# Performance work log

Hardware: AMD Instinct MI355X
Metric: run time of the kernel (lower is better)

## Reference

```python
import jax, jax.numpy as jnp
import numpy as np

N_NODES = 50000
N_EDGES = 800000
D_IN = 256
DIM_H = 256
N_GRAPHS = 500
N_OUT = 10
BN_EPS = 1e-5


def _mlp(h, W1, b1, gamma, beta, mean, var, W2, b2):
    # Linear -> BatchNorm1d (eval, running stats) -> ReLU -> Linear -> ReLU
    h = h @ W1 + b1
    h = (h - mean) * (gamma / jnp.sqrt(var + BN_EPS)) + beta
    h = jax.nn.relu(h)
    return jax.nn.relu(h @ W2 + b2)


def _gin_conv(x, src, dst, params):
    # PyG GINConv with eps=0: out = nn(x + sum_{j in N(i)} x_j)
    agg = jax.ops.segment_sum(x[src], dst, num_segments=N_NODES)
    return _mlp(x + agg, *params)


def setup_inputs() -> dict:
    key = jax.random.key(0)
    ks = jax.random.split(key, 24)
    x = jax.random.normal(ks[0], (N_NODES, D_IN), dtype=jnp.float32)
    edge_index = jax.random.randint(ks[1], (2, N_EDGES), 0, N_NODES, dtype=jnp.int64)
    batch = jnp.sort(jax.random.randint(ks[2], (N_NODES,), 0, N_GRAPHS, dtype=jnp.int64))

    def lin(k, fan_in, fan_out):
        s = 1.0 / np.sqrt(fan_in)
        kw, kb = jax.random.split(k)
        W = jax.random.uniform(kw, (fan_in, fan_out), minval=-s, maxval=s, dtype=jnp.float32)
        b = jax.random.uniform(kb, (fan_out,), minval=-s, maxval=s, dtype=jnp.float32)
        return W, b

    def bn(k, d):
        k1, k2, k3, k4 = jax.random.split(k, 4)
        gamma = 1.0 + 0.1 * jax.random.normal(k1, (d,), dtype=jnp.float32)
        beta = 0.1 * jax.random.normal(k2, (d,), dtype=jnp.float32)
        mean = 0.1 * jax.random.normal(k3, (d,), dtype=jnp.float32)
        var = jax.random.uniform(k4, (d,), minval=0.5, maxval=1.5, dtype=jnp.float32)
        return gamma, beta, mean, var

    W1a, b1a = lin(ks[3], D_IN, DIM_H)
    g1a, be1a, m1a, v1a = bn(ks[4], DIM_H)
    W2a, b2a = lin(ks[5], DIM_H, DIM_H)
    W1b, b1b = lin(ks[6], DIM_H, DIM_H)
    g1b, be1b, m1b, v1b = bn(ks[7], DIM_H)
    W2b, b2b = lin(ks[8], DIM_H, DIM_H)
    lin1_W, lin1_b = lin(ks[9], DIM_H * 2, DIM_H * 3)
    lin2_W, lin2_b = lin(ks[10], DIM_H * 3, N_OUT)

    return dict(x=x, edge_index=edge_index, batch=batch,
                W1a=W1a, b1a=b1a, g1a=g1a, be1a=be1a, m1a=m1a, v1a=v1a, W2a=W2a, b2a=b2a,
                W1b=W1b, b1b=b1b, g1b=g1b, be1b=be1b, m1b=m1b, v1b=v1b, W2b=W2b, b2b=b2b,
                lin1_W=lin1_W, lin1_b=lin1_b, lin2_W=lin2_W, lin2_b=lin2_b)


def reference(x, edge_index, batch,
              W1a, b1a, g1a, be1a, m1a, v1a, W2a, b2a,
              W1b, b1b, g1b, be1b, m1b, v1b, W2b, b2b,
              lin1_W, lin1_b, lin2_W, lin2_b):
    src, dst = edge_index[0], edge_index[1]
    h1 = _gin_conv(x, src, dst, (W1a, b1a, g1a, be1a, m1a, v1a, W2a, b2a))
    h2 = _gin_conv(h1, src, dst, (W1b, b1b, g1b, be1b, m1b, v1b, W2b, b2b))
    p1 = jax.ops.segment_sum(h1, batch, num_segments=N_GRAPHS)  # global_add_pool
    p2 = jax.ops.segment_sum(h2, batch, num_segments=N_GRAPHS)
    h = jnp.concatenate([p1, p2], axis=1)
    h = jax.nn.relu(h @ lin1_W + lin1_b)
    # dropout p=0.6 is identity in eval mode
    h = h @ lin2_W + lin2_b
    return jax.nn.log_softmax(h, axis=1)
```

## Files before the change

kernel.cpp:

```cpp
#include <hip/hip_runtime.h>

#define N_NODES 50000
#define MPAD 50176
#define N_EDGES 800000
#define DIM 256
#define N_GRAPHS 500
#define N_OUT 10
#define BN_EPS 1e-5f
#define SCAN_BS 1024
#define KSPLIT 4

typedef unsigned int u32;
typedef short bf16x8 __attribute__((ext_vector_type(8)));
typedef unsigned short us8 __attribute__((ext_vector_type(8)));
typedef float f32x4 __attribute__((ext_vector_type(4)));

typedef __attribute__((address_space(1))) const unsigned int gas_u32;
typedef __attribute__((address_space(3))) unsigned int las_u32;

__device__ inline void g2l16(const void* g, void* l) {
    __builtin_amdgcn_global_load_lds((gas_u32*)g, (las_u32*)l, 16, 0, 0);
}

__device__ inline float b2f(unsigned short u) {
    union { u32 i; float f; } c; c.i = ((u32)u) << 16; return c.f;
}
__device__ inline unsigned short f2b(float f) {
    u32 x = __builtin_bit_cast(u32, f);
    return (unsigned short)((x + 0x7FFFu + ((x >> 16) & 1u)) >> 16);
}

__global__ void zero_i(int* __restrict__ p, int n) {
    int i = blockIdx.x * blockDim.x + threadIdx.x;
    if (i < n) p[i] = 0;
}
__global__ void hist_dst(const int* __restrict__ dst, int* __restrict__ deg) {
    int e = blockIdx.x * blockDim.x + threadIdx.x;
    if (e < N_EDGES) atomicAdd(&deg[dst[e]], 1);
}
__global__ void scan_phase1(const int* __restrict__ deg, int* __restrict__ rowptr,
                            int* __restrict__ bsum, int n) {
    __shared__ int sh[SCAN_BS];
    int i = blockIdx.x * SCAN_BS + threadIdx.x;
    int v = (i < n) ? deg[i] : 0;
    sh[threadIdx.x] = v;
    __syncthreads();
    for (int off = 1; off < SCAN_BS; off <<= 1) {
        int t = (threadIdx.x >= off) ? sh[threadIdx.x - off] : 0;
        __syncthreads();
        sh[threadIdx.x] += t;
        __syncthreads();
    }
    if (i < n) rowptr[i] = sh[threadIdx.x] - v;
    if (threadIdx.x == SCAN_BS - 1) bsum[blockIdx.x] = sh[threadIdx.x];
}
__global__ void scan_phase2(int* __restrict__ bsum, int nb) {
    if (threadIdx.x == 0 && blockIdx.x == 0) {
        int run = 0;
        for (int b = 0; b < nb; b++) { int v = bsum[b]; bsum[b] = run; run += v; }
    }
}
__global__ void scan_phase3(int* __restrict__ rowptr, int* __restrict__ cursor,
                            const int* __restrict__ bsum, int n) {
    int i = blockIdx.x * SCAN_BS + threadIdx.x;
    if (i < n) {
        int v = rowptr[i] + bsum[blockIdx.x];
        rowptr[i] = v;
        cursor[i] = v;
    }
    if (i == 0) rowptr[n] = N_EDGES;
}
__global__ void fill_csr(const int* __restrict__ src, const int* __restrict__ dst,
                         int* __restrict__ cursor, int* __restrict__ col) {
    int e = blockIdx.x * blockDim.x + threadIdx.x;
    if (e < N_EDGES) {
        int p = atomicAdd(&cursor[dst[e]], 1);
        col[p] = src[e];
    }
}
__global__ void graph_starts(const int* __restrict__ batch, int* __restrict__ gstart) {
    int g = blockIdx.x * blockDim.x + threadIdx.x;
    if (g > N_GRAPHS) return;
    if (g == N_GRAPHS) { gstart[g] = N_NODES; return; }
    int lo = 0, hi = N_NODES;
    while (lo < hi) { int mid = (lo + hi) >> 1; if (batch[mid] < g) lo = mid + 1; else hi = mid; }
    gstart[g] = lo;
}

__global__ void conv_x(const float4* __restrict__ in, ushort4* __restrict__ out, int n4) {
    int i = blockIdx.x * blockDim.x + threadIdx.x;
    if (i < n4) {
        float4 v = in[i];
        ushort4 o; o.x = f2b(v.x); o.y = f2b(v.y); o.z = f2b(v.z); o.w = f2b(v.w);
        out[i] = o;
    }
}
__global__ void conv_wt4(const float* __restrict__ W0, const float* __restrict__ W1,
                         const float* __restrict__ W2, const float* __restrict__ W3,
                         unsigned short* __restrict__ Wt) {
    int mat = blockIdx.y;
    const float* W = (mat == 0) ? W0 : (mat == 1) ? W1 : (mat == 2) ? W2 : W3;
    int n = blockIdx.x;
    int k = threadIdx.x;
    Wt[((size_t)mat << 16) + (size_t)n * 256 + k] = f2b(W[(size_t)k * 256 + n]);
}
__global__ void make_ss(const float* __restrict__ bias, const float* __restrict__ gamma,
                        const float* __restrict__ beta, const float* __restrict__ mean,
                        const float* __restrict__ var, float* __restrict__ scale,
                        float* __restrict__ shift, int has_bn) {
    int i = threadIdx.x;
    if (has_bn) {
        float s = gamma[i] * rsqrtf(var[i] + BN_EPS);
        scale[i] = s;
        shift[i] = (bias[i] - mean[i]) * s + beta[i];
    } else {
        scale[i] = 1.f;
        shift[i] = bias[i];
    }
}

__global__ void gather_bf(const unsigned short* __restrict__ feat,
                          const int* __restrict__ col,
                          const int* __restrict__ rowptr,
                          unsigned short* __restrict__ out) {
    int node = blockIdx.x * 4 + (threadIdx.x >> 6);
    if (node >= N_NODES) return;
    int lane = threadIdx.x & 63;
    int half = lane >> 5;
    int d8 = (lane & 31) * 8;
    float acc[8];
    #pragma unroll
    for (int j = 0; j < 8; j++) acc[j] = 0.f;
    if (half == 0) {
        us8 own = *reinterpret_cast<const us8*>(&feat[(size_t)node * DIM + d8]);
        #pragma unroll
        for (int j = 0; j < 8; j++) acc[j] = b2f((unsigned short)own[j]);
    }
    int s = rowptr[node], e = rowptr[node + 1];
    int i = s + half;
    for (; i + 6 < e; i += 8) {
        int n0 = col[i], n1 = col[i + 2], n2 = col[i + 4], n3 = col[i + 6];
        us8 v0 = *reinterpret_cast<const us8*>(&feat[(size_t)n0 * DIM + d8]);
        us8 v1 = *reinterpret_cast<const us8*>(&feat[(size_t)n1 * DIM + d8]);
        us8 v2 = *reinterpret_cast<const us8*>(&feat[(size_t)n2 * DIM + d8]);
        us8 v3 = *reinterpret_cast<const us8*>(&feat[(size_t)n3 * DIM + d8]);
        #pragma unroll
        for (int j = 0; j < 8; j++)
            acc[j] += (b2f((unsigned short)v0[j]) + b2f((unsigned short)v1[j]))
                    + (b2f((unsigned short)v2[j]) + b2f((unsigned short)v3[j]));
    }
    for (; i < e; i += 2) {
        int n0 = col[i];
        us8 v0 = *reinterpret_cast<const us8*>(&feat[(size_t)n0 * DIM + d8]);
        #pragma unroll
        for (int j = 0; j < 8; j++) acc[j] += b2f((unsigned short)v0[j]);
    }
    #pragma unroll
    for (int j = 0; j < 8; j++) acc[j] += __shfl_xor(acc[j], 32, 64);
    if (half == 0) {
        us8 o;
        #pragma unroll
        for (int j = 0; j < 8; j++) o[j] = (short)f2b(acc[j]);
        *reinterpret_cast<us8*>(&out[(size_t)node * DIM + d8]) = o;
    }
}

__global__ __launch_bounds__(512)
void gemm_bf16(const unsigned short* __restrict__ A,
               const unsigned short* __restrict__ Wt,
               const float* __restrict__ scale,
               const float* __restrict__ shift,
               unsigned short* __restrict__ C, int M) {
    __shared__ unsigned short Asb[2][128 * 32];
    __shared__ unsigned short Bsb[2][256 * 32];
    int t = threadIdx.x;
    int wave = t >> 6, lane = t & 63;
    int m0 = blockIdx.x * 128;
    int wr = (wave >> 2) * 64;
    int wc = (wave & 3) * 64;

    int cb = (t & 3) * 16;
    const char* Ab  = (const char*)A  + (size_t)(m0 + (t >> 2)) * 512 + cb;
    const char* Bb0 = (const char*)Wt + (size_t)(t >> 2) * 512 + cb;
    const char* Bb1 = (const char*)Wt + (size_t)(128 + (t >> 2)) * 512 + cb;

    f32x4 acc[4][4];
    #pragma unroll
    for (int m = 0; m < 4; m++)
        #pragma unroll
        for (int n = 0; n < 4; n++)
            acc[m][n] = (f32x4){0.f, 0.f, 0.f, 0.f};

    int rsel = lane & 15;
    int ksel = (lane >> 4) * 8;

    #pragma unroll
    for (int p = 0; p < 2; p++) {
        size_t ko = (size_t)p * 64;
        g2l16(Ab + ko,  (char*)Asb[p] + (size_t)t * 16);
        g2l16(Bb0 + ko, (char*)Bsb[p] + (size_t)t * 16);
        g2l16(Bb1 + ko, (char*)Bsb[p] + (size_t)(512 + t) * 16);
    }

    #pragma unroll
    for (int ks = 0; ks < 8; ks++) {
        const int cur = ks & 1;
        if (ks < 7) asm volatile("s_waitcnt vmcnt(3)" ::: "memory");
        else        asm volatile("s_waitcnt vmcnt(0)" ::: "memory");
        __builtin_amdgcn_s_barrier();
        asm volatile("" ::: "memory");

        const unsigned short* As = Asb[cur];
        const unsigned short* Bs = Bsb[cur];
        bf16x8 af[4], bfr[4];
        #pragma unroll
        for (int m = 0; m < 4; m++)
            af[m] = *(const bf16x8*)&As[(size_t)(wr + m * 16 + rsel) * 32 + ksel];
        #pragma unroll
        for (int n = 0; n < 4; n++)
            bfr[n] = *(const bf16x8*)&Bs[(size_t)(wc + n * 16 + rsel) * 32 + ksel];
        #pragma unroll
        for (int m = 0; m < 4; m++)
            #pragma unroll
            for (int n = 0; n < 4; n++)
                acc[m][n] = __builtin_amdgcn_mfma_f32_16x16x32_bf16(af[m], bfr[n], acc[m][n], 0, 0, 0);

        asm volatile("" ::: "memory");
        __builtin_amdgcn_s_barrier();
        if (ks + 2 < 8) {
            size_t ko = (size_t)(ks + 2) * 64;
            g2l16(Ab + ko,  (char*)Asb[cur] + (size_t)t * 16);
            g2l16(Bb0 + ko, (char*)Bsb[cur] + (size_t)t * 16);
            g2l16(Bb1 + ko, (char*)Bsb[cur] + (size_t)(512 + t) * 16);
        }
    }

    int cr = lane >> 4;
    #pragma unroll
    for (int n = 0; n < 4; n++) {
        int colg = wc + n * 16 + rsel;
        float s = scale[colg], sh = shift[colg];
        #pragma unroll
        for (int m = 0; m < 4; m++) {
            int rowb = m0 + wr + m * 16 + cr * 4;
            #pragma unroll
            for (int r = 0; r < 4; r++) {
                int row = rowb + r;
                if (row < M) {
                    float v = fmaxf(acc[m][n][r] * s + sh, 0.f);
                    C[(size_t)row * 256 + colg] = f2b(v);
                }
            }
        }
    }
}

__global__ void pool_seg(const unsigned short* __restrict__ h1,
                         const unsigned short* __restrict__ h2,
                         const int* __restrict__ gstart,
                         float* __restrict__ pcat) {
    int g = blockIdx.x;
    int t = threadIdx.x;
    int s = gstart[g], e = gstart[g + 1];
    float a1 = 0.f, a2 = 0.f;
    for (int n = s; n < e; n++) {
        a1 += b2f(h1[(size_t)n * DIM + t]);
        a2 += b2f(h2[(size_t)n * DIM + t]);
    }
    pcat[(size_t)g * 512 + t]       = a1;
    pcat[(size_t)g * 512 + 256 + t] = a2;
}

__global__ void head1(const float* __restrict__ A,
                      const float* __restrict__ W1,
                      float* __restrict__ Hpart) {
    __shared__ float As[16][65];
    __shared__ float Bs[16][65];
    int t = threadIdx.x;
    int m0 = blockIdx.y * 64;
    int n0 = blockIdx.x * 64;
    int kz = blockIdx.z * (512 / KSPLIT);
    int tx = t & 15, ty = t >> 4;
    float acc[4][4] = {};
    for (int k0 = kz; k0 < kz + 512 / KSPLIT; k0 += 16) {
        #pragma unroll
        for (int i = 0; i < 4; i++) {
            int r = (t >> 4) + i * 16;
            int k = t & 15;
            int gr = m0 + r;
            As[k][r] = (gr < N_GRAPHS) ? A[(size_t)gr * 512 + k0 + k] : 0.f;
        }
        #pragma unroll
        for (int i = 0; i < 4; i++) {
            int k = (t >> 6) + i * 4;
            int n = t & 63;
            Bs[k][n] = W1[(size_t)(k0 + k) * 768 + n0 + n];
        }
        __syncthreads();
        #pragma unroll
        for (int k = 0; k < 16; k++) {
            float a[4], b[4];
            #pragma unroll
            for (int i = 0; i < 4; i++) a[i] = As[k][ty * 4 + i];
            #pragma unroll
            for (int j = 0; j < 4; j++) b[j] = Bs[k][tx * 4 + j];
            #pragma unroll
            for (int i = 0; i < 4; i++)
                #pragma unroll
                for (int j = 0; j < 4; j++)
                    acc[i][j] += a[i] * b[j];
        }
        __syncthreads();
    }
    float* Hz = Hpart + (size_t)blockIdx.z * N_GRAPHS * 768;
    #pragma unroll
    for (int i = 0; i < 4; i++) {
        int gm = m0 + ty * 4 + i;
        if (gm >= N_GRAPHS) continue;
        #pragma unroll
        for (int j = 0; j < 4; j++) {
            int gn = n0 + tx * 4 + j;
            Hz[(size_t)gm * 768 + gn] = acc[i][j];
        }
    }
}

__global__ void head2(const float* __restrict__ Hpart, const float* __restrict__ b1,
                      const float* __restrict__ W2, const float* __restrict__ b2,
                      float* __restrict__ out) {
    int g = blockIdx.x;
    int lane = threadIdx.x;
    float part[N_OUT];
    #pragma unroll
    for (int o = 0; o < N_OUT; o++) part[o] = 0.f;
    for (int k = lane; k < 768; k += 64) {
        float hv = b1[k];
        #pragma unroll
        for (int z = 0; z < KSPLIT; z++)
            hv += Hpart[((size_t)z * N_GRAPHS + g) * 768 + k];
        hv = fmaxf(hv, 0.f);
        #pragma unroll
        for (int o = 0; o < N_OUT; o++) part[o] += hv * W2[(size_t)k * N_OUT + o];
    }
    #pragma unroll
    for (int o = 0; o < N_OUT; o++) {
        #pragma unroll
        for (int off = 32; off > 0; off >>= 1)
            part[o] += __shfl_down(part[o], off, 64);
    }
    if (lane == 0) {
        float logits[N_OUT];
        float mx = -1e30f;
        #pragma unroll
        for (int o = 0; o < N_OUT; o++) { logits[o] = part[o] + b2[o]; mx = fmaxf(mx, logits[o]); }
        float ssum = 0.f;
        #pragma unroll
        for (int o = 0; o < N_OUT; o++) ssum += expf(logits[o] - mx);
        float lse = logf(ssum);
        #pragma unroll
        for (int o = 0; o < N_OUT; o++)
            out[(size_t)g * N_OUT + o] = logits[o] - mx - lse;
    }
}

extern "C" void kernel_launch(void* const* d_in, const int* in_sizes, int n_in,
                              void* d_out, int out_size, void* d_ws, size_t ws_size,
                              hipStream_t stream) {
    const float* x     = (const float*)d_in[0];
    const int*   ei    = (const int*)d_in[1];
    const int*   batch = (const int*)d_in[2];
    const float* W1a = (const float*)d_in[3];
    const float* b1a = (const float*)d_in[4];
    const float* g1a = (const float*)d_in[5];
    const float* be1a= (const float*)d_in[6];
    const float* m1a = (const float*)d_in[7];
    const float* v1a = (const float*)d_in[8];
    const float* W2a = (const float*)d_in[9];
    const float* b2a = (const float*)d_in[10];
    const float* W1b = (const float*)d_in[11];
    const float* b1b = (const float*)d_in[12];
    const float* g1b = (const float*)d_in[13];
    const float* be1b= (const float*)d_in[14];
    const float* m1b = (const float*)d_in[15];
    const float* v1b = (const float*)d_in[16];
    const float* W2b = (const float*)d_in[17];
    const float* b2b = (const float*)d_in[18];
    const float* lin1_W = (const float*)d_in[19];
    const float* lin1_b = (const float*)d_in[20];
    const float* lin2_W = (const float*)d_in[21];
    const float* lin2_b = (const float*)d_in[22];

    const size_t NBUF = (size_t)MPAD * DIM;
    char* ws = (char*)d_ws;
    unsigned short* agg  = (unsigned short*)ws;            ws += NBUF * 2;
    unsigned short* mid  = (unsigned short*)ws;            ws += NBUF * 2;
    unsigned short* h1   = (unsigned short*)ws;            ws += NBUF * 2;
    unsigned short* h2   = (unsigned short*)ws;            ws += NBUF * 2;
    unsigned short* x_bf = (unsigned short*)ws;            ws += (size_t)N_NODES * DIM * 2;
    unsigned short* Wt   = (unsigned short*)ws;            ws += 4 * 65536 * 2;
    float* ss    = (float*)ws;                             ws += 8 * 256 * 4;
    float* pcat  = (float*)ws;                             ws += (size_t)N_GRAPHS * 512 * 4;
    float* Hpart = (float*)ws;                             ws += (size_t)KSPLIT * N_GRAPHS * 768 * 4;
    int* deg     = (int*)ws;                               ws += (size_t)N_NODES * 4;
    int* cursor  = (int*)ws;                               ws += (size_t)N_NODES * 4;
    int* rowptr  = (int*)ws;                               ws += (size_t)(N_NODES + 1) * 4;
    int* bsum    = (int*)ws;                               ws += 64 * 4;
    int* col     = (int*)ws;                               ws += (size_t)N_EDGES * 4;
    int* gstart  = (int*)ws;

    const int* srcE = ei;
    const int* dstE = ei + N_EDGES;

    const int nscan = (N_NODES + SCAN_BS - 1) / SCAN_BS;

    zero_i<<<(N_NODES + 255) / 256, 256, 0, stream>>>(deg, N_NODES);
    hist_dst<<<(N_EDGES + 255) / 256, 256, 0, stream>>>(dstE, deg);
    scan_phase1<<<nscan, SCAN_BS, 0, stream>>>(deg, rowptr, bsum, N_NODES);
    scan_phase2<<<1, 64, 0, stream>>>(bsum, nscan);
    scan_phase3<<<nscan, SCAN_BS, 0, stream>>>(rowptr, cursor, bsum, N_NODES);
    fill_csr<<<(N_EDGES + 255) / 256, 256, 0, stream>>>(srcE, dstE, cursor, col);
    graph_starts<<<2, 256, 0, stream>>>(batch, gstart);

    conv_x<<<(N_NODES * DIM / 4 + 255) / 256, 256, 0, stream>>>(
        (const float4*)x, (ushort4*)x_bf, N_NODES * DIM / 4);
    dim3 wt_grid(256, 4);
    conv_wt4<<<wt_grid, 256, 0, stream>>>(W1a, W2a, W1b, W2b, Wt);
    make_ss<<<1, 256, 0, stream>>>(b1a, g1a, be1a, m1a, v1a, ss + 0 * 512, ss + 0 * 512 + 256, 1);
    make_ss<<<1, 256, 0, stream>>>(b2a, nullptr, nullptr, nullptr, nullptr, ss + 1 * 512, ss + 1 * 512 + 256, 0);
    make_ss<<<1, 256, 0, stream>>>(b1b, g1b, be1b, m1b, v1b, ss + 2 * 512, ss + 2 * 512 + 256, 1);
    make_ss<<<1, 256, 0, stream>>>(b2b, nullptr, nullptr, nullptr, nullptr, ss + 3 * 512, ss + 3 * 512 + 256, 0);

    gather_bf<<<(N_NODES + 3) / 4, 256, 0, stream>>>(x_bf, col, rowptr, agg);
    gemm_bf16<<<MPAD / 128, 512, 0, stream>>>(agg, Wt + 0 * 65536, ss + 0 * 512, ss + 0 * 512 + 256, mid, N_NODES);
    gemm_bf16<<<MPAD / 128, 512, 0, stream>>>(mid, Wt + 1 * 65536, ss + 1 * 512, ss + 1 * 512 + 256, h1, N_NODES);

    gather_bf<<<(N_NODES + 3) / 4, 256, 0, stream>>>(h1, col, rowptr, agg);
    gemm_bf16<<<MPAD / 128, 512, 0, stream>>>(agg, Wt + 2 * 65536, ss + 2 * 512, ss + 2 * 512 + 256, mid, N_NODES);
    gemm_bf16<<<MPAD / 128, 512, 0, stream>>>(mid, Wt + 3 * 65536, ss + 3 * 512, ss + 3 * 512 + 256, h2, N_NODES);

    pool_seg<<<N_GRAPHS, 256, 0, stream>>>(h1, h2, gstart, pcat);
    dim3 h1grid(12, 8, KSPLIT);
    head1<<<h1grid, 256, 0, stream>>>(pcat, lin1_W, Hpart);
    head2<<<N_GRAPHS, 64, 0, stream>>>(Hpart, lin1_b, lin2_W, lin2_b, (float*)d_out);
}
```

Before: 395.3 us.

## Fuse both MLP GEMMs into one kernel keeping intermediate tile in LDS

Replaces the two back-to-back GEMM launches per GIN layer with a single kernel that computes Linear+BN+ReLU into a swizzled LDS buffer, then runs the second GEMM straight from LDS. This removes the global write and re-read of the 50k x 256 intermediate activation and one launch per layer, and it prefetches the second weight matrix during the tail of the first GEMM. In exchange, tiles shrink from 128 to 64 rows with 4 waves, each block reloads both full weight matrices, and LDS use grows to about 72 KB, which may limit occupancy.

```diff
diff --git a/kernel.cpp b/kernel.cpp
--- a/kernel.cpp
+++ b/kernel.cpp
@@ -28,6 +28,10 @@
 __device__ inline unsigned short f2b(float f) {
     u32 x = __builtin_bit_cast(u32, f);
     return (unsigned short)((x + 0x7FFFu + ((x >> 16) & 1u)) >> 16);
+}
+
+__device__ inline int mid_addr(int row, int col) {
+    return row * 512 + ((((col >> 3) ^ (row & 31)) << 4) | ((col & 7) << 1));
 }
 
 __global__ void zero_i(int* __restrict__ p, int n) {
@@ -107,16 +111,11 @@
 __global__ void make_ss(const float* __restrict__ bias, const float* __restrict__ gamma,
                         const float* __restrict__ beta, const float* __restrict__ mean,
                         const float* __restrict__ var, float* __restrict__ scale,
-                        float* __restrict__ shift, int has_bn) {
+                        float* __restrict__ shift) {
     int i = threadIdx.x;
-    if (has_bn) {
-        float s = gamma[i] * rsqrtf(var[i] + BN_EPS);
-        scale[i] = s;
-        shift[i] = (bias[i] - mean[i]) * s + beta[i];
-    } else {
-        scale[i] = 1.f;
-        shift[i] = bias[i];
-    }
+    float s = gamma[i] * rsqrtf(var[i] + BN_EPS);
+    scale[i] = s;
+    shift[i] = (bias[i] - mean[i]) * s + beta[i];
 }
 
 __global__ void gather_bf(const unsigned short* __restrict__ feat,
@@ -165,24 +164,39 @@
     }
 }
 
-__global__ __launch_bounds__(512)
-void gemm_bf16(const unsigned short* __restrict__ A,
-               const unsigned short* __restrict__ Wt,
-               const float* __restrict__ scale,
-               const float* __restrict__ shift,
-               unsigned short* __restrict__ C, int M) {
-    __shared__ unsigned short Asb[2][128 * 32];
-    __shared__ unsigned short Bsb[2][256 * 32];
+__global__ __launch_bounds__(256, 2)
+void fused_mlp(const unsigned short* __restrict__ A,
+               const unsigned short* __restrict__ W1t,
+               const unsigned short* __restrict__ W2t,
+               const float* __restrict__ scale1,
+               const float* __restrict__ shift1,
+               const float* __restrict__ shift2,
+               unsigned short* __restrict__ H, int M) {
+    __shared__ __align__(16) unsigned short Asb[2][64 * 32];
+    __shared__ __align__(16) unsigned short Bsb[2][256 * 32];
+    __shared__ __align__(16) unsigned short midb[64 * 256];
+
     int t = threadIdx.x;
     int wave = t >> 6, lane = t & 63;
-    int m0 = blockIdx.x * 128;
-    int wr = (wave >> 2) * 64;
-    int wc = (wave & 3) * 64;
+    int m0 = blockIdx.x * 64;
+    int wc = wave * 64;
+    int rsel = lane & 15;
+    int ksel = (lane >> 4) * 8;
+    int cr = lane >> 4;
+
+    float s1[4], sh1[4], sh2[4];
+    #pragma unroll
+    for (int n = 0; n < 4; n++) {
+        int colg = wc + n * 16 + rsel;
+        s1[n]  = scale1[colg];
+        sh1[n] = shift1[colg];
+        sh2[n] = shift2[colg];
+    }
 
     int cb = (t & 3) * 16;
-    const char* Ab  = (const char*)A  + (size_t)(m0 + (t >> 2)) * 512 + cb;
-    const char* Bb0 = (const char*)Wt + (size_t)(t >> 2) * 512 + cb;
-    const char* Bb1 = (const char*)Wt + (size_t)(128 + (t >> 2)) * 512 + cb;
+    const char* Ab  = (const char*)A   + (size_t)(m0 + (t >> 2)) * 512 + cb;
+    const char* B1b = (const char*)W1t + (size_t)(t >> 2) * 512 + cb;
+    const char* B2b = (const char*)W2t + (size_t)(t >> 2) * 512 + cb;
 
     f32x4 acc[4][4];
     #pragma unroll
@@ -191,22 +205,20 @@
         for (int n = 0; n < 4; n++)
             acc[m][n] = (f32x4){0.f, 0.f, 0.f, 0.f};
 
-    int rsel = lane & 15;
-    int ksel = (lane >> 4) * 8;
-
     #pragma unroll
     for (int p = 0; p < 2; p++) {
         size_t ko = (size_t)p * 64;
-        g2l16(Ab + ko,  (char*)Asb[p] + (size_t)t * 16);
-        g2l16(Bb0 + ko, (char*)Bsb[p] + (size_t)t * 16);
-        g2l16(Bb1 + ko, (char*)Bsb[p] + (size_t)(512 + t) * 16);
+        g2l16(Ab + ko, (char*)Asb[p] + (size_t)t * 16);
+        #pragma unroll
+        for (int i = 0; i < 4; i++)
+            g2l16(B1b + (size_t)i * 32768 + ko, (char*)Bsb[p] + (size_t)(i * 256 + t) * 16);
     }
 
     #pragma unroll
     for (int ks = 0; ks < 8; ks++) {
         const int cur = ks & 1;
-        if (ks < 7) asm volatile("s_waitcnt vmcnt(3)" ::: "memory");
-        else        asm volatile("s_waitcnt vmcnt(0)" ::: "memory");
+        if (ks < 7) asm volatile("s_waitcnt vmcnt(5)" ::: "memory");
+        else        asm volatile("s_waitcnt vmcnt(4)" ::: "memory");
         __builtin_amdgcn_s_barrier();
         asm volatile("" ::: "memory");
 
@@ -215,7 +227,7 @@
         bf16x8 af[4], bfr[4];
         #pragma unroll
         for (int m = 0; m < 4; m++)
-            af[m] = *(const bf16x8*)&As[(size_t)(wr + m * 16 + rsel) * 32 + ksel];
+            af[m] = *(const bf16x8*)&As[(size_t)(m * 16 + rsel) * 32 + ksel];
         #pragma unroll
         for (int n = 0; n < 4; n++)
             bfr[n] = *(const bf16x8*)&Bs[(size_t)(wc + n * 16 + rsel) * 32 + ksel];
@@ -229,26 +241,83 @@
         __builtin_amdgcn_s_barrier();
         if (ks + 2 < 8) {
             size_t ko = (size_t)(ks + 2) * 64;
-            g2l16(Ab + ko,  (char*)Asb[cur] + (size_t)t * 16);
-            g2l16(Bb0 + ko, (char*)Bsb[cur] + (size_t)t * 16);
-            g2l16(Bb1 + ko, (char*)Bsb[cur] + (size_t)(512 + t) * 16);
-        }
-    }
-
-    int cr = lane >> 4;
+            g2l16(Ab + ko, (char*)Asb[cur] + (size_t)t * 16);
+            #pragma unroll
+            for (int i = 0; i < 4; i++)
+                g2l16(B1b + (size_t)i * 32768 + ko, (char*)Bsb[cur] + (size_t)(i * 256 + t) * 16);
+        } else if (ks == 6) {
+            #pragma unroll
+            for (int i = 0; i < 4; i++)
+                g2l16(B2b + (size_t)i * 32768, (char*)Bsb[0] + (size_t)(i * 256 + t) * 16);
+        } else {
+            #pragma unroll
+            for (int i = 0; i < 4; i++)
+                g2l16(B2b + (size_t)i * 32768 + 64, (char*)Bsb[1] + (size_t)(i * 256 + t) * 16);
+        }
+    }
+
     #pragma unroll
     for (int n = 0; n < 4; n++) {
         int colg = wc + n * 16 + rsel;
-        float s = scale[colg], sh = shift[colg];
         #pragma unroll
         for (int m = 0; m < 4; m++) {
-            int rowb = m0 + wr + m * 16 + cr * 4;
+            int rowb = m * 16 + cr * 4;
+            #pragma unroll
+            for (int r = 0; r < 4; r++) {
+                float v = fmaxf(acc[m][n][r] * s1[n] + sh1[n], 0.f);
+                *(unsigned short*)((char*)midb + mid_addr(rowb + r, colg)) = f2b(v);
+                acc[m][n][r] = 0.f;
+            }
+        }
+    }
+    asm volatile("s_waitcnt lgkmcnt(0)" ::: "memory");
+    __builtin_amdgcn_s_barrier();
+    asm volatile("" ::: "memory");
+
+    #pragma unroll
+    for (int ks = 0; ks < 8; ks++) {
+        const int cur = ks & 1;
+        if (ks < 7) asm volatile("s_waitcnt vmcnt(4)" ::: "memory");
+        else        asm volatile("s_waitcnt vmcnt(0)" ::: "memory");
+        __builtin_amdgcn_s_barrier();
+        asm volatile("" ::: "memory");
+
+        const unsigned short* Bs = Bsb[cur];
+        bf16x8 af[4], bfr[4];
+        #pragma unroll
+        for (int m = 0; m < 4; m++)
+            af[m] = *(const bf16x8*)((const char*)midb + mid_addr(m * 16 + rsel, ks * 32 + ksel));
+        #pragma unroll
+        for (int n = 0; n < 4; n++)
+            bfr[n] = *(const bf16x8*)&Bs[(size_t)(wc + n * 16 + rsel) * 32 + ksel];
+        #pragma unroll
+        for (int m = 0; m < 4; m++)
+            #pragma unroll
+            for (int n = 0; n < 4; n++)
+                acc[m][n] = __builtin_amdgcn_mfma_f32_16x16x32_bf16(af[m], bfr[n], acc[m][n], 0, 0, 0);
+
+        asm volatile("" ::: "memory");
+        __builtin_amdgcn_s_barrier();
+        if (ks + 2 < 8) {
+            size_t ko = (size_t)(ks + 2) * 64;
+            #pragma unroll
+            for (int i = 0; i < 4; i++)
+                g2l16(B2b + (size_t)i * 32768 + ko, (char*)Bsb[cur] + (size_t)(i * 256 + t) * 16);
+        }
+    }
+
+    #pragma unroll
+    for (int n = 0; n < 4; n++) {
+        int colg = wc + n * 16 + rsel;
+        #pragma unroll
+        for (int m = 0; m < 4; m++) {
+            int rowb = m0 + m * 16 + cr * 4;
             #pragma unroll
             for (int r = 0; r < 4; r++) {
                 int row = rowb + r;
                 if (row < M) {
-                    float v = fmaxf(acc[m][n][r] * s + sh, 0.f);
-                    C[(size_t)row * 256 + colg] = f2b(v);
+                    float v = fmaxf(acc[m][n][r] + sh2[n], 0.f);
+                    H[(size_t)row * 256 + colg] = f2b(v);
                 }
             }
         }
@@ -393,12 +462,11 @@
     const size_t NBUF = (size_t)MPAD * DIM;
     char* ws = (char*)d_ws;
     unsigned short* agg  = (unsigned short*)ws;            ws += NBUF * 2;
-    unsigned short* mid  = (unsigned short*)ws;            ws += NBUF * 2;
     unsigned short* h1   = (unsigned short*)ws;            ws += NBUF * 2;
     unsigned short* h2   = (unsigned short*)ws;            ws += NBUF * 2;
     unsigned short* x_bf = (unsigned short*)ws;            ws += (size_t)N_NODES * DIM * 2;
     unsigned short* Wt   = (unsigned short*)ws;            ws += 4 * 65536 * 2;
-    float* ss    = (float*)ws;                             ws += 8 * 256 * 4;
+    float* ss    = (float*)ws;                             ws += 4 * 256 * 4;
     float* pcat  = (float*)ws;                             ws += (size_t)N_GRAPHS * 512 * 4;
     float* Hpart = (float*)ws;                             ws += (size_t)KSPLIT * N_GRAPHS * 768 * 4;
     int* deg     = (int*)ws;                               ws += (size_t)N_NODES * 4;
@@ -425,18 +493,16 @@
         (const float4*)x, (ushort4*)x_bf, N_NODES * DIM / 4);
     dim3 wt_grid(256, 4);
     conv_wt4<<<wt_grid, 256, 0, stream>>>(W1a, W2a, W1b, W2b, Wt);
-    make_ss<<<1, 256, 0, stream>>>(b1a, g1a, be1a, m1a, v1a, ss + 0 * 512, ss + 0 * 512 + 256, 1);
-    make_ss<<<1, 256, 0, stream>>>(b2a, nullptr, nullptr, nullptr, nullptr, ss + 1 * 512, ss + 1 * 512 + 256, 0);
-    make_ss<<<1, 256, 0, stream>>>(b1b, g1b, be1b, m1b, v1b, ss + 2 * 512, ss + 2 * 512 + 256, 1);
-    make_ss<<<1, 256, 0, stream>>>(b2b, nullptr, nullptr, nullptr, nullptr, ss + 3 * 512, ss + 3 * 512 + 256, 0);
+    make_ss<<<1, 256, 0, stream>>>(b1a, g1a, be1a, m1a, v1a, ss + 0 * 512, ss + 0 * 512 + 256);
+    make_ss<<<1, 256, 0, stream>>>(b1b, g1b, be1b, m1b, v1b, ss + 1 * 512, ss + 1 * 512 + 256);
 
     gather_bf<<<(N_NODES + 3) / 4, 256, 0, stream>>>(x_bf, col, rowptr, agg);
-    gemm_bf16<<<MPAD / 128, 512, 0, stream>>>(agg, Wt + 0 * 65536, ss + 0 * 512, ss + 0 * 512 + 256, mid, N_NODES);
-    gemm_bf16<<<MPAD / 128, 512, 0, stream>>>(mid, Wt + 1 * 65536, ss + 1 * 512, ss + 1 * 512 + 256, h1, N_NODES);
+    fused_mlp<<<MPAD / 64, 256, 0, stream>>>(agg, Wt + 0 * 65536, Wt + 1 * 65536,
+                                             ss + 0 * 512, ss + 0 * 512 + 256, b2a, h1, N_NODES);
 
     gather_bf<<<(N_NODES + 3) / 4, 256, 0, stream>>>(h1, col, rowptr, agg);
-    gemm_bf16<<<MPAD / 128, 512, 0, stream>>>(agg, Wt + 2 * 65536, ss + 2 * 512, ss + 2 * 512 + 256, mid, N_NODES);
-    gemm_bf16<<<MPAD / 128, 512, 0, stream>>>(mid, Wt + 3 * 65536, ss + 3 * 512, ss + 3 * 512 + 256, h2, N_NODES);
+    fused_mlp<<<MPAD / 64, 256, 0, stream>>>(agg, Wt + 2 * 65536, Wt + 3 * 65536,
+                                             ss + 1 * 512, ss + 1 * 512 + 256, b2b, h2, N_NODES);
 
     pool_seg<<<N_GRAPHS, 256, 0, stream>>>(h1, h2, gstart, pcat);
     dim3 h1grid(12, 8, KSPLIT);
```

Result: faster. 365.4 us (-7.6%).
